# Optimization experiments

Measured on AMD Instinct MI355X. Metric: run time of the kernel, lower is better.

The kernel has to match this reference:

```python
import jax, jax.numpy as jnp
import numpy as np

N = 100_000      # nodes
F_IN = 256       # num_features
HID = 128        # args.hidden
C = 32           # num_classes
E = 1_600_000    # edges
EPS = 0.1        # AntiSymmetricConv epsilon
GAMMA = 0.1      # AntiSymmetricConv gamma


def setup_inputs() -> dict:
    key = jax.random.key(0)
    ks = jax.random.split(key, 10)
    def rn(k, shape, scale=0.05):
        return jax.random.normal(k, shape, dtype=jnp.float32) * scale
    x = jax.random.normal(ks[0], (N, F_IN), dtype=jnp.float32)
    edge_index = jax.random.randint(ks[1], (2, E), 0, N, dtype=jnp.int32)
    return {
        "x": x,
        "lin1_w": rn(ks[2], (HID, F_IN)), "lin1_b": jnp.zeros((HID,), jnp.float32),
        "lin2_w": rn(ks[3], (C, HID)),   "lin2_b": jnp.zeros((C,), jnp.float32),
        "W1": rn(ks[4], (HID, HID)), "phi1_w": rn(ks[5], (HID, HID)), "b1": jnp.zeros((HID,), jnp.float32),
        "W2": rn(ks[6], (C, C)),     "phi2_w": rn(ks[7], (C, C)),     "b2": jnp.zeros((C,), jnp.float32),
        "edge_index": edge_index,
    }


def gcn_norm(edge_index, n):
    # GCNConv default: add self-loops, symmetric D^-1/2 (A+I) D^-1/2 normalization
    loops = jnp.arange(n, dtype=edge_index.dtype)
    row = jnp.concatenate([edge_index[0], loops])  # source
    col = jnp.concatenate([edge_index[1], loops])  # target (aggregation)
    deg = jax.ops.segment_sum(jnp.ones(row.shape[0], jnp.float32), col, num_segments=n)
    dinv = jnp.where(deg > 0, jax.lax.rsqrt(deg), 0.0)
    return row, col, dinv[row] * dinv[col]


def gcn_conv(x, phi_w, row, col, norm):
    xw = x @ phi_w.T                                  # [N, d]
    msgs = norm[:, None] * xw[row]                    # [E+N, d] gather
    return jax.ops.segment_sum(msgs, col, num_segments=x.shape[0])  # scatter-add


def anti_symmetric_conv(x, row, col, norm, W, phi_w, b):
    d = W.shape[0]
    aw = W - W.T - GAMMA * jnp.eye(d, dtype=W.dtype)  # antisymmetric weight
    h = gcn_conv(x, phi_w, row, col, norm)            # phi(x, edge_index)
    h = jnp.tanh(x @ aw.T + h + b)
    return x + EPS * h                                # one Euler step (num_iters=1)


def reference(x, lin1_w, lin1_b, lin2_w, lin2_b, W1, phi1_w, b1, W2, phi2_w, b2, edge_index):
    row, col, norm = gcn_norm(edge_index, x.shape[0])
    h = jax.nn.relu(x @ lin1_w.T + lin1_b)            # dropout is identity in eval
    h = anti_symmetric_conv(h, row, col, norm, W1, phi1_w, b1)
    h = h @ lin2_w.T + lin2_b
    h = anti_symmetric_conv(h, row, col, norm, W2, phi2_w, b2)
    return jax.nn.log_softmax(h, axis=1)
```

## Files before the change

kernel.cpp:

```cpp
#include <hip/hip_runtime.h>
#include <hip/hip_bf16.h>
#include <math.h>

#define N_NODES 100000
#define F_IN    256
#define HID     128
#define NCLS    32
#define NEDGES  1600000
#define EPS_C   0.1f
#define GAMMA_C 0.1f

#define NBK   782
#define CHUNK 4096
#define NCH   391
#define BMAX  4096

typedef __attribute__((ext_vector_type(8))) short short8;
typedef __attribute__((ext_vector_type(4))) float floatx4;

__device__ __forceinline__ float bf2f(unsigned short u) {
    union { unsigned int u; float f; } c;
    c.u = ((unsigned int)u) << 16;
    return c.f;
}
__device__ __forceinline__ unsigned short f2bf(float f) {
    union { float f; unsigned int u; } c; c.f = f;
    unsigned int u = c.u;
    u += 0x7FFFu + ((u >> 16) & 1u);
    return (unsigned short)(u >> 16);
}

__device__ __forceinline__ short8 cvt8(float4 u, float4 v) {
    short8 r;
    r[0] = (short)f2bf(u.x); r[1] = (short)f2bf(u.y);
    r[2] = (short)f2bf(u.z); r[3] = (short)f2bf(u.w);
    r[4] = (short)f2bf(v.x); r[5] = (short)f2bf(v.y);
    r[6] = (short)f2bf(v.z); r[7] = (short)f2bf(v.w);
    return r;
}

__device__ __forceinline__ float ldf(const void* p, size_t i, int md) {
    return md ? ((const float*)p)[i] : bf2f(((const unsigned short*)p)[i]);
}

__global__ void k_detect(const unsigned short* __restrict__ x, int* __restrict__ mode) {
    __shared__ int cnt;
    if (threadIdx.x == 0) cnt = 0;
    __syncthreads();
    float v = fabsf(bf2f(x[2 * threadIdx.x]));
    if (v > 1e4f || !isfinite(v)) atomicAdd(&cnt, 1);
    __syncthreads();
    if (threadIdx.x == 0) *mode = (cnt >= 8) ? 1 : 0;
}

__global__ __launch_bounds__(256) void k_cvtx(const void* __restrict__ x,
                                              unsigned short* __restrict__ xbf,
                                              const int* __restrict__ dmode, int n8) {
    if (!dmode[0]) return;
    const float* xf = (const float*)x;
    int stride = gridDim.x * 256;
    for (int i = blockIdx.x * 256 + threadIdx.x; i < n8; i += stride) {
        const float* q = xf + (size_t)i * 8;
        float4 u = *(const float4*)q, v = *(const float4*)(q + 4);
        *(short8*)(xbf + (size_t)i * 8) = cvt8(u, v);
    }
}

__global__ __launch_bounds__(256) void k_cvtw(const void* __restrict__ w1,
                                              const void* __restrict__ w2,
                                              const void* __restrict__ w3,
                                              const void* __restrict__ w4,
                                              unsigned short* __restrict__ out,
                                              const int* __restrict__ dmode) {
    if (!dmode[0]) return;
    int i = blockIdx.x * 256 + threadIdx.x;
    const float* src; int off;
    if (i < 4096)      { src = (const float*)w1; off = i; }
    else if (i < 6144) { src = (const float*)w2; off = i - 4096; }
    else if (i < 6656) { src = (const float*)w3; off = i - 6144; }
    else if (i < 6784) { src = (const float*)w4; off = i - 6656; }
    else return;
    const float* q = src + (size_t)off * 8;
    *(short8*)(out + (size_t)i * 8) = cvt8(*(const float4*)q, *(const float4*)(q + 4));
}

__global__ __launch_bounds__(256) void k_hist2(const int* __restrict__ ecol,
                                               int* __restrict__ hist, int e) {
    __shared__ int lh[NBK];
    for (int i = threadIdx.x; i < NBK; i += 256) lh[i] = 0;
    __syncthreads();
    int base = blockIdx.x * CHUNK;
    int lim = base + CHUNK; if (lim > e) lim = e;
    for (int i = base + threadIdx.x; i < lim; i += 256)
        atomicAdd(&lh[ecol[i] >> 7], 1);
    __syncthreads();
    for (int i = threadIdx.x; i < NBK; i += 256) hist[blockIdx.x * NBK + i] = lh[i];
}

__global__ __launch_bounds__(256) void k_tot(const int* __restrict__ hist, int* __restrict__ tot) {
    __shared__ int s[256];
    int b = blockIdx.x;
    int v = 0;
    for (int blk = threadIdx.x; blk < NCH; blk += 256) v += hist[blk * NBK + b];
    s[threadIdx.x] = v;
    __syncthreads();
#pragma unroll
    for (int off = 128; off > 0; off >>= 1) {
        if (threadIdx.x < off) s[threadIdx.x] += s[threadIdx.x + off];
        __syncthreads();
    }
    if (threadIdx.x == 0) tot[b] = s[0];
}

__global__ void k_bscan(const int* __restrict__ tot, int* __restrict__ bbase) {
    __shared__ int s[1024];
    int v = (threadIdx.x < NBK) ? tot[threadIdx.x] : 0;
    s[threadIdx.x] = v;
    __syncthreads();
#pragma unroll
    for (int off = 1; off < 1024; off <<= 1) {
        int t = (threadIdx.x >= off) ? s[threadIdx.x - off] : 0;
        __syncthreads();
        s[threadIdx.x] += t;
        __syncthreads();
    }
    if (threadIdx.x < NBK) bbase[threadIdx.x] = s[threadIdx.x] - v;
}

__global__ __launch_bounds__(512) void k_colscan(const int* __restrict__ hist,
                                                 const int* __restrict__ bbase,
                                                 int* __restrict__ off) {
    __shared__ int s[512];
    int b = blockIdx.x, t = threadIdx.x;
    int v = (t < NCH) ? hist[t * NBK + b] : 0;
    s[t] = v;
    __syncthreads();
#pragma unroll
    for (int o = 1; o < 512; o <<= 1) {
        int u = (t >= o) ? s[t - o] : 0;
        __syncthreads();
        s[t] += u;
        __syncthreads();
    }
    if (t < NCH) off[t * NBK + b] = s[t] - v + bbase[b];
}

__global__ __launch_bounds__(256) void k_pass3(
    const int* __restrict__ erow, const int* __restrict__ ecol,
    const int* __restrict__ off, unsigned int* __restrict__ pairs, int e)
{
    __shared__ int lh[NBK];
    __shared__ int lex[NBK + 1];
    __shared__ int cur[NBK];
    __shared__ int wsum[256];
    __shared__ unsigned int sp[CHUNK];
    int base = blockIdx.x * CHUNK;
    int lim = base + CHUNK; if (lim > e) lim = e;
    int cnt = lim - base;

    for (int i = threadIdx.x; i < NBK; i += 256) lh[i] = 0;
    __syncthreads();
    for (int i = base + threadIdx.x; i < lim; i += 256)
        atomicAdd(&lh[ecol[i] >> 7], 1);
    __syncthreads();

    int t4 = threadIdx.x * 4;
    int a0 = (t4 + 0 < NBK) ? lh[t4 + 0] : 0;
    int a1 = (t4 + 1 < NBK) ? lh[t4 + 1] : 0;
    int a2 = (t4 + 2 < NBK) ? lh[t4 + 2] : 0;
    int a3 = (t4 + 3 < NBK) ? lh[t4 + 3] : 0;
    int mysum = a0 + a1 + a2 + a3;
    wsum[threadIdx.x] = mysum;
    __syncthreads();
#pragma unroll
    for (int o = 1; o < 256; o <<= 1) {
        int u = (threadIdx.x >= o) ? wsum[threadIdx.x - o] : 0;
        __syncthreads();
        wsum[threadIdx.x] += u;
        __syncthreads();
    }
    int run = wsum[threadIdx.x] - mysum;
    if (t4 + 0 < NBK) { lex[t4 + 0] = run;            cur[t4 + 0] = run; }
    if (t4 + 1 < NBK) { lex[t4 + 1] = run + a0;       cur[t4 + 1] = run + a0; }
    if (t4 + 2 < NBK) { lex[t4 + 2] = run + a0 + a1;  cur[t4 + 2] = run + a0 + a1; }
    if (t4 + 3 < NBK) { lex[t4 + 3] = run + a0 + a1 + a2; cur[t4 + 3] = run + a0 + a1 + a2; }
    if (threadIdx.x == 0) lex[NBK] = cnt;
    __syncthreads();

    for (int i = base + threadIdx.x; i < lim; i += 256) {
        int dst = ecol[i], src = erow[i];
        int b = dst >> 7;
        int p = atomicAdd(&cur[b], 1);
        sp[p] = ((unsigned int)src << 7) | (unsigned int)(dst & 127);
    }
    __syncthreads();

    for (int i = threadIdx.x; i < cnt; i += 256) {
        int loB = 0, hiB = NBK;
        while (hiB - loB > 1) {
            int mid = (loB + hiB) >> 1;
            if (lex[mid] <= i) loB = mid; else hiB = mid;
        }
        pairs[off[blockIdx.x * NBK + loB] + (i - lex[loB])] = sp[i];
    }
}

__global__ __launch_bounds__(256) void k_build(
    const int* __restrict__ tot, const int* __restrict__ bbase,
    const unsigned int* __restrict__ pairs,
    int* __restrict__ srt, int* __restrict__ row_start, int* __restrict__ cend,
    float* __restrict__ dinv, int n)
{
    __shared__ int lh[128];
    __shared__ int lo[128];
    __shared__ unsigned int se[BMAX];
    int b = blockIdx.x;
    int nb = tot[b]; if (nb > BMAX) nb = BMAX;
    int base = bbase[b];
    if (threadIdx.x < 128) lh[threadIdx.x] = 0;
    __syncthreads();
    for (int e = threadIdx.x; e < nb; e += 256) {
        unsigned int pk = pairs[(size_t)base + e];
        se[e] = pk;
        atomicAdd(&lh[pk & 127u], 1);
    }
    __syncthreads();
    if (threadIdx.x < 128) lo[threadIdx.x] = lh[threadIdx.x];
    __syncthreads();
#pragma unroll
    for (int off = 1; off < 128; off <<= 1) {
        int t = (threadIdx.x < 128 && threadIdx.x >= off) ? lo[threadIdx.x - off] : 0;
        __syncthreads();
        if (threadIdx.x < 128) lo[threadIdx.x] += t;
        __syncthreads();
    }
    int node = b * 128 + threadIdx.x;
    if (threadIdx.x < 128 && node < n) {
        int inc = lo[threadIdx.x], cnt = lh[threadIdx.x];
        row_start[node] = base + inc - cnt;
        cend[node]      = base + inc;
        dinv[node]      = rsqrtf((float)cnt + 1.0f);
    }
    __syncthreads();
    if (threadIdx.x < 128) lh[threadIdx.x] = lo[threadIdx.x] - lh[threadIdx.x];
    __syncthreads();
    for (int e = threadIdx.x; e < nb; e += 256) {
        unsigned int pk = se[e];
        int pos = atomicAdd(&lh[pk & 127u], 1);
        srt[base + pos] = (int)(pk >> 7);
    }
}

__global__ void k_aw(const void* __restrict__ W, unsigned short* __restrict__ aw,
                     const int* __restrict__ dmode, int d) {
    int idx = blockIdx.x * blockDim.x + threadIdx.x;
    if (idx >= d * d) return;
    int md = dmode[0];
    int n = idx / d, k = idx - n * d;
    float v = ldf(W, n * d + k, md) - ldf(W, k * d + n, md) - ((n == k) ? GAMMA_C : 0.0f);
    aw[idx] = f2bf(v);
}

template<int K, int NCB, int NCF, int EPI, int NSPLIT, bool ASEL, bool BSEL>
__global__ __launch_bounds__(512) void k_gemm6(
    const void* A, const unsigned short* Acvt,
    const void* B, const unsigned short* Bcvt, const void* bias,
    unsigned short* Cout,
    const unsigned short* agg, const unsigned short* xw, const float* dinv,
    const int* dmode, void* opout, int M)
{
    constexpr int KP = K + 8;
    constexpr int NT = NCB / 16;
    constexpr int KS = K / 32;
    constexpr int SN = (NCB * K) / 4096;
    __shared__ __align__(16) unsigned short sB[NCB * KP];
    const int md = dmode[0];

    const unsigned short* Ab = (ASEL && md) ? Acvt : (const unsigned short*)A;
    const unsigned short* Bb = (BSEL && md) ? Bcvt : (const unsigned short*)B;

    const int rowblk = (NSPLIT > 1) ? ((int)blockIdx.x / NSPLIT) : (int)blockIdx.x;
    const int col0   = (NSPLIT > 1) ? ((int)blockIdx.x % NSPLIT) * NCB : 0;

    const int lane = threadIdx.x & 63;
    const int wave = threadIdx.x >> 6;
    const int l15  = lane & 15;
    const int quad = lane >> 4;
    const int row0 = rowblk * 128 + wave * 16;

    int ar = row0 + l15;
    int am = ar < M ? ar : M - 1;

    short8 a[KS];
#pragma unroll
    for (int s = 0; s < KS; ++s)
        a[s] = *(const short8*)(Ab + (size_t)am * K + s * 32 + quad * 8);

    if constexpr (SN >= 1) {
        short8 st[SN];
#pragma unroll
        for (int i = 0; i < SN; ++i) {
            int base = threadIdx.x * 8 + i * 4096;
            int r = base / K, c = base % K;
            st[i] = *(const short8*)(Bb + (size_t)(col0 + r) * K + c);
        }
#pragma unroll
        for (int i = 0; i < SN; ++i) {
            int base = threadIdx.x * 8 + i * 4096;
            int r = base / K, c = base % K;
            *(short8*)(sB + r * KP + c) = st[i];
        }
    } else {
        if (threadIdx.x < (NCB * K) / 8) {
            int base = threadIdx.x * 8;
            int r = base / K, c = base % K;
            *(short8*)(sB + r * KP + c) =
                *(const short8*)(Bb + (size_t)(col0 + r) * K + c);
        }
    }
    __builtin_amdgcn_sched_barrier(0);
    __syncthreads();

    floatx4 acc[NT];
#pragma unroll
    for (int t = 0; t < NT; ++t) acc[t] = (floatx4){0.f, 0.f, 0.f, 0.f};

#pragma unroll
    for (int s = 0; s < KS; ++s) {
        short8 b[NT];
#pragma unroll
        for (int t = 0; t < NT; ++t)
            b[t] = *(const short8*)(sB + (t * 16 + l15) * KP + s * 32 + quad * 8);
#pragma unroll
        for (int t = 0; t < NT; ++t)
            acc[t] = __builtin_amdgcn_mfma_f32_16x16x32_bf16(a[s], b[t], acc[t], 0, 0, 0);
    }

    const unsigned short* Ares = Ab;
#pragma unroll
    for (int reg = 0; reg < 4; ++reg) {
        int rr = row0 + quad * 4 + reg;
        if (EPI == 4) {
            int rrc = rr < M ? rr : M - 1;
            float dv = dinv[rrc];
            float val[NT];
#pragma unroll
            for (int t = 0; t < NT; ++t) {
                int col = t * 16 + l15;
                float z = acc[t][reg]
                        + bf2f(agg[(size_t)rrc * NCF + col])
                        + dv * bf2f(xw[(size_t)rrc * NCF + col])
                        + ldf(bias, col, md);
                val[t] = bf2f(Ares[(size_t)rrc * K + col]) + EPS_C * tanhf(z);
            }
            float m = val[0];
#pragma unroll
            for (int t = 1; t < NT; ++t) m = fmaxf(m, val[t]);
#pragma unroll
            for (int msk = 1; msk < 16; msk <<= 1) m = fmaxf(m, __shfl_xor(m, msk));
            float s = 0.f;
#pragma unroll
            for (int t = 0; t < NT; ++t) s += expf(val[t] - m);
#pragma unroll
            for (int msk = 1; msk < 16; msk <<= 1) s += __shfl_xor(s, msk);
            float ls = m + logf(s);
            if (rr < M) {
#pragma unroll
                for (int t = 0; t < NT; ++t) {
                    int col = t * 16 + l15;
                    float r = val[t] - ls;
                    if (md) ((float*)opout)[(size_t)rr * NCF + col] = r;
                    else    ((unsigned short*)opout)[(size_t)rr * NCF + col] = f2bf(r);
                }
            }
        } else {
            if (rr >= M) continue;
#pragma unroll
            for (int t = 0; t < NT; ++t) {
                int gcol = col0 + t * 16 + l15;
                float v = acc[t][reg];
                if (EPI == 0) { v += ldf(bias, gcol, md); v = v > 0.f ? v : 0.f; }
                else if (EPI == 5) { v *= dinv[rr]; }
                else if (EPI == 3) {
                    float dv = dinv[rr];
                    float z = v + bf2f(agg[(size_t)rr * NCF + gcol])
                            + dv * bf2f(xw[(size_t)rr * NCF + gcol])
                            + ldf(bias, gcol, md);
                    v = bf2f(Ares[(size_t)rr * K + gcol]) + EPS_C * tanhf(z);
                }
                Cout[(size_t)rr * NCF + gcol] = f2bf(v);
            }
        }
    }
}

__global__ __launch_bounds__(256) void k_lin2phi2(
    const unsigned short* __restrict__ A,
    const void* __restrict__ B1, const unsigned short* __restrict__ B1c,
    const void* __restrict__ bias,
    const void* __restrict__ B2, const unsigned short* __restrict__ B2c,
    unsigned short* __restrict__ h3, unsigned short* __restrict__ xws2,
    const float* __restrict__ dinv, const int* __restrict__ dmode, int M)
{
    constexpr int K1 = 128, KP1 = 136, KP2 = 40;
    __shared__ __align__(16) unsigned short sB1[32 * KP1];
    __shared__ __align__(16) unsigned short sB2[32 * KP2];
    __shared__ __align__(16) unsigned short sT[128 * KP2];
    const int md = dmode[0];

    const unsigned short* B1b = md ? B1c : (const unsigned short*)B1;
    const unsigned short* B2b = md ? B2c : (const unsigned short*)B2;

    const int lane = threadIdx.x & 63;
    const int wave = threadIdx.x >> 6;
    const int l15  = lane & 15;
    const int quad = lane >> 4;
    const int row0 = blockIdx.x * 128 + wave * 32;

    int am[2];
#pragma unroll
    for (int rt = 0; rt < 2; ++rt) {
        int r = row0 + rt * 16 + l15;
        am[rt] = r < M ? r : M - 1;
    }

    short8 a1[4][2];
#pragma unroll
    for (int s = 0; s < 4; ++s)
#pragma unroll
        for (int rt = 0; rt < 2; ++rt)
            a1[s][rt] = *(const short8*)(A + (size_t)am[rt] * K1 + s * 32 + quad * 8);

    short8 s1[2], s2;
    const bool has2 = threadIdx.x * 8 < 1024;
#pragma unroll
    for (int i = 0; i < 2; ++i)
        s1[i] = *(const short8*)(B1b + threadIdx.x * 8 + i * 2048);
    if (has2)
        s2 = *(const short8*)(B2b + threadIdx.x * 8);
#pragma unroll
    for (int i = 0; i < 2; ++i) {
        int base = threadIdx.x * 8 + i * 2048;
        int r = base / K1, c = base - r * K1;
        *(short8*)(sB1 + r * KP1 + c) = s1[i];
    }
    if (has2) {
        int base = threadIdx.x * 8;
        int r = base / 32, c = base - r * 32;
        *(short8*)(sB2 + r * KP2 + c) = s2;
    }
    __builtin_amdgcn_sched_barrier(0);
    __syncthreads();

    floatx4 acc[2][2];
#pragma unroll
    for (int rt = 0; rt < 2; ++rt) { acc[rt][0] = (floatx4){0,0,0,0}; acc[rt][1] = (floatx4){0,0,0,0}; }

#pragma unroll
    for (int s = 0; s < 4; ++s) {
#pragma unroll
        for (int rt = 0; rt < 2; ++rt) {
#pragma unroll
            for (int t = 0; t < 2; ++t) {
                short8 b = *(const short8*)(sB1 + (t * 16 + l15) * KP1 + s * 32 + quad * 8);
                acc[rt][t] = __builtin_amdgcn_mfma_f32_16x16x32_bf16(a1[s][rt], b, acc[rt][t], 0, 0, 0);
            }
        }
    }
#pragma unroll
    for (int rt = 0; rt < 2; ++rt)
#pragma unroll
        for (int reg = 0; reg < 4; ++reg) {
            int rr = row0 + rt * 16 + quad * 4 + reg;
            int lr = wave * 32 + rt * 16 + quad * 4 + reg;
#pragma unroll
            for (int t = 0; t < 2; ++t) {
                int col = t * 16 + l15;
                unsigned short hv = f2bf(acc[rt][t][reg] + ldf(bias, col, md));
                sT[lr * KP2 + col] = hv;
                if (rr < M) h3[(size_t)rr * 32 + col] = hv;
            }
        }
    __syncthreads();

    floatx4 a2[2][2];
#pragma unroll
    for (int rt = 0; rt < 2; ++rt) {
        short8 a = *(const short8*)(sT + (wave * 32 + rt * 16 + l15) * KP2 + quad * 8);
#pragma unroll
        for (int t = 0; t < 2; ++t) {
            short8 b = *(const short8*)(sB2 + (t * 16 + l15) * KP2 + quad * 8);
            a2[rt][t] = __builtin_amdgcn_mfma_f32_16x16x32_bf16(a, b, (floatx4){0,0,0,0}, 0, 0, 0);
        }
    }
#pragma unroll
    for (int rt = 0; rt < 2; ++rt)
#pragma unroll
        for (int reg = 0; reg < 4; ++reg) {
            int rr = row0 + rt * 16 + quad * 4 + reg;
            if (rr >= M) continue;
            float dv = dinv[rr];
#pragma unroll
            for (int t = 0; t < 2; ++t)
                xws2[(size_t)rr * 32 + t * 16 + l15] = f2bf(dv * a2[rt][t][reg]);
        }
}

__global__ __launch_bounds__(256) void k_gather128(
    const int* __restrict__ srt, const int* __restrict__ rs,
    const int* __restrict__ cend,
    const unsigned short* __restrict__ xws, const float* __restrict__ dinv,
    unsigned short* __restrict__ agg, int n)
{
    int node = blockIdx.x * 8 + (threadIdx.x >> 5);
    int l = threadIdx.x & 31;
    if (node >= n) return;
    int j = rs[node], end = cend[node];
    float a0 = 0.f, a1 = 0.f, a2 = 0.f, a3 = 0.f;
    while (j < end) {
        int idx[8];
#pragma unroll
        for (int k = 0; k < 8; ++k) {
            int jj = j + k;
            idx[k] = srt[jj < end ? jj : end - 1];
        }
        uint2 p[8];
#pragma unroll
        for (int k = 0; k < 8; ++k)
            p[k] = *(const uint2*)(xws + (size_t)idx[k] * 128 + l * 4);
#pragma unroll
        for (int k = 0; k < 8; ++k) {
            if (j + k < end) {
                a0 += bf2f((unsigned short)(p[k].x & 0xFFFFu));
                a1 += bf2f((unsigned short)(p[k].x >> 16));
                a2 += bf2f((unsigned short)(p[k].y & 0xFFFFu));
                a3 += bf2f((unsigned short)(p[k].y >> 16));
            }
        }
        j += 8;
    }
    float dn = dinv[node];
    uint2 out;
    out.x = (unsigned int)f2bf(dn * a0) | ((unsigned int)f2bf(dn * a1) << 16);
    out.y = (unsigned int)f2bf(dn * a2) | ((unsigned int)f2bf(dn * a3) << 16);
    *(uint2*)(agg + (size_t)node * 128 + l * 4) = out;
}

__global__ __launch_bounds__(256) void k_gather32(
    const int* __restrict__ srt, const int* __restrict__ rs,
    const int* __restrict__ cend,
    const unsigned short* __restrict__ xws, const float* __restrict__ dinv,
    unsigned short* __restrict__ agg, int n)
{
    int node = blockIdx.x * 16 + (threadIdx.x >> 4);
    int l = threadIdx.x & 15;
    if (node >= n) return;
    int j = rs[node], end = cend[node];
    float a0 = 0.f, a1 = 0.f;
    while (j < end) {
        int idx[8];
#pragma unroll
        for (int k = 0; k < 8; ++k) {
            int jj = j + k;
            idx[k] = srt[jj < end ? jj : end - 1];
        }
        unsigned int p[8];
#pragma unroll
        for (int k = 0; k < 8; ++k)
            p[k] = *(const unsigned int*)(xws + (size_t)idx[k] * 32 + l * 2);
#pragma unroll
        for (int k = 0; k < 8; ++k) {
            if (j + k < end) {
                a0 += bf2f((unsigned short)(p[k] & 0xFFFFu));
                a1 += bf2f((unsigned short)(p[k] >> 16));
            }
        }
        j += 8;
    }
    float dn = dinv[node];
    unsigned int out = (unsigned int)f2bf(dn * a0) | ((unsigned int)f2bf(dn * a1) << 16);
    *(unsigned int*)(agg + (size_t)node * 32 + l * 2) = out;
}

extern "C" void kernel_launch(void* const* d_in, const int* in_sizes, int n_in,
                              void* d_out, int out_size, void* d_ws, size_t ws_size,
                              hipStream_t stream)
{
    const void* x      = d_in[0];
    const void* lin1_w = d_in[1];
    const void* lin1_b = d_in[2];
    const void* lin2_w = d_in[3];
    const void* lin2_b = d_in[4];
    const void* W1     = d_in[5];
    const void* phi1w  = d_in[6];
    const void* b1     = d_in[7];
    const void* W2     = d_in[8];
    const void* phi2w  = d_in[9];
    const void* b2     = d_in[10];
    const int* eidx    = (const int*)d_in[11];
    const int* erow = eidx;
    const int* ecol = eidx + NEDGES;

    char* ws = (char*)d_ws;
    float* dinv          = (float*)ws;
    int*   dmode         = (int*)(ws + 400000);
    unsigned short* aw1  = (unsigned short*)(ws + 401408);
    unsigned short* aw2  = (unsigned short*)(ws + 435200);
    int* tot             = (int*)(ws + 440320);
    int* bbase           = (int*)(ws + 443648);
    int* row_start       = (int*)(ws + 446976);
    int* cend            = (int*)(ws + 846976);
    int* srt             = (int*)(ws + 1246976);
    int* hist            = (int*)(ws + 7646976);
    int* offb            = (int*)(ws + 8870912);
    unsigned short* wbf  = (unsigned short*)(ws + 10094080);
    unsigned short* h1   = (unsigned short*)(ws + 10485760);
    unsigned short* xws1 = h1 + (size_t)N_NODES * HID;
    unsigned short* agg1 = xws1 + (size_t)N_NODES * HID;
    unsigned short* h2   = xws1;
    unsigned short* h3   = h1;
    unsigned short* xws2 = agg1;
    unsigned short* agg2 = agg1 + (size_t)N_NODES * NCLS;
    unsigned int* pairs  = (unsigned int*)agg1;
    unsigned short* xbf  = xws1;

    unsigned short* bw1 = wbf;
    unsigned short* bp1 = wbf + 32768;
    unsigned short* bw2 = wbf + 49152;
    unsigned short* bp2 = wbf + 53248;

    const int GB = 256;
    const int NB5 = (N_NODES + 127) / 128;
    k_detect<<<1, 256, 0, stream>>>((const unsigned short*)x, dmode);

    k_hist2<<<NCH, 256, 0, stream>>>(ecol, hist, NEDGES);
    k_tot<<<NBK, 256, 0, stream>>>(hist, tot);
    k_bscan<<<1, 1024, 0, stream>>>(tot, bbase);
    k_colscan<<<NBK, 512, 0, stream>>>(hist, bbase, offb);
    k_pass3<<<NCH, 256, 0, stream>>>(erow, ecol, offb, pairs, NEDGES);
    k_build<<<NBK, 256, 0, stream>>>(tot, bbase, pairs, srt, row_start, cend, dinv, N_NODES);

    k_aw<<<(HID * HID + GB - 1) / GB, GB, 0, stream>>>(W1, aw1, dmode, HID);
    k_aw<<<(NCLS * NCLS + GB - 1) / GB, GB, 0, stream>>>(W2, aw2, dmode, NCLS);
    k_cvtw<<<27, 256, 0, stream>>>(lin1_w, phi1w, lin2_w, phi2w, wbf, dmode);
    k_cvtx<<<2048, 256, 0, stream>>>(x, xbf, dmode, N_NODES * F_IN / 8);

    k_gemm6<256, 64, 128, 0, 2, true, true><<<NB5 * 2, 512, 0, stream>>>(
        x, xbf, lin1_w, bw1, lin1_b, h1, nullptr, nullptr, nullptr, dmode, nullptr, N_NODES);
    k_gemm6<128, 128, 128, 5, 1, false, true><<<NB5, 512, 0, stream>>>(
        h1, nullptr, phi1w, bp1, nullptr, xws1, nullptr, nullptr, dinv, dmode, nullptr, N_NODES);
    k_gather128<<<(N_NODES + 7) / 8, 256, 0, stream>>>(
        srt, row_start, cend, xws1, dinv, agg1, N_NODES);
    k_gemm6<128, 128, 128, 3, 1, false, false><<<NB5, 512, 0, stream>>>(
        h1, nullptr, aw1, nullptr, b1, h2, agg1, xws1, dinv, dmode, nullptr, N_NODES);
    k_lin2phi2<<<(N_NODES + 127) / 128, 256, 0, stream>>>(
        h2, lin2_w, bw2, lin2_b, phi2w, bp2, h3, xws2, dinv, dmode, N_NODES);
    k_gather32<<<(N_NODES + 15) / 16, 256, 0, stream>>>(
        srt, row_start, cend, xws2, dinv, agg2, N_NODES);
    k_gemm6<32, 32, 32, 4, 1, false, false><<<NB5, 512, 0, stream>>>(
        h3, nullptr, aw2, nullptr, b2, nullptr, agg2, xws2, dinv, dmode, d_out, N_NODES);
}
```

Baseline: 435.6 us.

## Store layer-1 phi features in column-sliced layout for narrower gathers

```diff
diff --git a/kernel.cpp b/kernel.cpp
--- a/kernel.cpp
+++ b/kernel.cpp
@@ -261,7 +261,8 @@
     aw[idx] = f2bf(v);
 }
 
-template<int K, int NCB, int NCF, int EPI, int NSPLIT, bool ASEL, bool BSEL>
+template<int K, int NCB, int NCF, int EPI, int NSPLIT, bool ASEL, bool BSEL,
+         bool SLCW, bool SLCR>
 __global__ __launch_bounds__(512) void k_gemm6(
     const void* A, const unsigned short* Acvt,
     const void* B, const unsigned short* Bcvt, const void* bias,
@@ -273,6 +274,7 @@
     constexpr int NT = NCB / 16;
     constexpr int KS = K / 32;
     constexpr int SN = (NCB * K) / 4096;
+    constexpr size_t N16 = (size_t)N_NODES * 16;
     __shared__ __align__(16) unsigned short sB[NCB * KP];
     const int md = dmode[0];
 
@@ -383,12 +385,16 @@
                 else if (EPI == 5) { v *= dinv[rr]; }
                 else if (EPI == 3) {
                     float dv = dinv[rr];
-                    float z = v + bf2f(agg[(size_t)rr * NCF + gcol])
-                            + dv * bf2f(xw[(size_t)rr * NCF + gcol])
+                    size_t aoff = SLCR ? ((size_t)t * N16 + (size_t)rr * 16 + l15)
+                                       : ((size_t)rr * NCF + gcol);
+                    float z = v + bf2f(agg[aoff])
+                            + dv * bf2f(xw[aoff])
                             + ldf(bias, gcol, md);
                     v = bf2f(Ares[(size_t)rr * K + gcol]) + EPS_C * tanhf(z);
                 }
-                Cout[(size_t)rr * NCF + gcol] = f2bf(v);
+                size_t coff = SLCW ? ((size_t)t * N16 + (size_t)rr * 16 + l15)
+                                   : ((size_t)rr * NCF + gcol);
+                Cout[coff] = f2bf(v);
             }
         }
     }
@@ -506,17 +512,20 @@
         }
 }
 
-__global__ __launch_bounds__(256) void k_gather128(
+__global__ __launch_bounds__(256) void k_gather128s(
     const int* __restrict__ srt, const int* __restrict__ rs,
     const int* __restrict__ cend,
-    const unsigned short* __restrict__ xws, const float* __restrict__ dinv,
-    unsigned short* __restrict__ agg, int n)
+    const unsigned short* __restrict__ xslc, const float* __restrict__ dinv,
+    unsigned short* __restrict__ aggs, int n)
 {
-    int node = blockIdx.x * 8 + (threadIdx.x >> 5);
-    int l = threadIdx.x & 31;
+    constexpr size_t N16 = (size_t)N_NODES * 16;
+    const int slice = blockIdx.x & 7;
+    const int node = (blockIdx.x >> 3) * 32 + (threadIdx.x >> 3);
+    const int l = threadIdx.x & 7;
     if (node >= n) return;
+    const unsigned short* xs = xslc + (size_t)slice * N16;
     int j = rs[node], end = cend[node];
-    float a0 = 0.f, a1 = 0.f, a2 = 0.f, a3 = 0.f;
+    float a0 = 0.f, a1 = 0.f;
     while (j < end) {
         int idx[8];
 #pragma unroll
@@ -524,26 +533,22 @@
             int jj = j + k;
             idx[k] = srt[jj < end ? jj : end - 1];
         }
-        uint2 p[8];
+        unsigned int p[8];
 #pragma unroll
         for (int k = 0; k < 8; ++k)
-            p[k] = *(const uint2*)(xws + (size_t)idx[k] * 128 + l * 4);
+            p[k] = *(const unsigned int*)(xs + (size_t)idx[k] * 16 + l * 2);
 #pragma unroll
         for (int k = 0; k < 8; ++k) {
             if (j + k < end) {
-                a0 += bf2f((unsigned short)(p[k].x & 0xFFFFu));
-                a1 += bf2f((unsigned short)(p[k].x >> 16));
-                a2 += bf2f((unsigned short)(p[k].y & 0xFFFFu));
-                a3 += bf2f((unsigned short)(p[k].y >> 16));
+                a0 += bf2f((unsigned short)(p[k] & 0xFFFFu));
+                a1 += bf2f((unsigned short)(p[k] >> 16));
             }
         }
         j += 8;
     }
     float dn = dinv[node];
-    uint2 out;
-    out.x = (unsigned int)f2bf(dn * a0) | ((unsigned int)f2bf(dn * a1) << 16);
-    out.y = (unsigned int)f2bf(dn * a2) | ((unsigned int)f2bf(dn * a3) << 16);
-    *(uint2*)(agg + (size_t)node * 128 + l * 4) = out;
+    unsigned int out = (unsigned int)f2bf(dn * a0) | ((unsigned int)f2bf(dn * a1) << 16);
+    *(unsigned int*)(aggs + (size_t)slice * N16 + (size_t)node * 16 + l * 2) = out;
 }
 
 __global__ __launch_bounds__(256) void k_gather32(
@@ -617,8 +622,8 @@
     unsigned short* h1   = (unsigned short*)(ws + 10485760);
     unsigned short* xws1 = h1 + (size_t)N_NODES * HID;
     unsigned short* agg1 = xws1 + (size_t)N_NODES * HID;
-    unsigned short* h2   = xws1;
-    unsigned short* h3   = h1;
+    unsigned short* h2   = h1;
+    unsigned short* h3   = xws1;
     unsigned short* xws2 = agg1;
     unsigned short* agg2 = agg1 + (size_t)N_NODES * NCLS;
     unsigned int* pairs  = (unsigned int*)agg1;
@@ -645,18 +650,18 @@
     k_cvtw<<<27, 256, 0, stream>>>(lin1_w, phi1w, lin2_w, phi2w, wbf, dmode);
     k_cvtx<<<2048, 256, 0, stream>>>(x, xbf, dmode, N_NODES * F_IN / 8);
 
-    k_gemm6<256, 64, 128, 0, 2, true, true><<<NB5 * 2, 512, 0, stream>>>(
+    k_gemm6<256, 64, 128, 0, 2, true, true, false, false><<<NB5 * 2, 512, 0, stream>>>(
         x, xbf, lin1_w, bw1, lin1_b, h1, nullptr, nullptr, nullptr, dmode, nullptr, N_NODES);
-    k_gemm6<128, 128, 128, 5, 1, false, true><<<NB5, 512, 0, stream>>>(
+    k_gemm6<128, 128, 128, 5, 1, false, true, true, false><<<NB5, 512, 0, stream>>>(
         h1, nullptr, phi1w, bp1, nullptr, xws1, nullptr, nullptr, dinv, dmode, nullptr, N_NODES);
-    k_gather128<<<(N_NODES + 7) / 8, 256, 0, stream>>>(
+    k_gather128s<<<(N_NODES / 32) * 8, 256, 0, stream>>>(
         srt, row_start, cend, xws1, dinv, agg1, N_NODES);
-    k_gemm6<128, 128, 128, 3, 1, false, false><<<NB5, 512, 0, stream>>>(
+    k_gemm6<128, 128, 128, 3, 1, false, false, false, true><<<NB5, 512, 0, stream>>>(
         h1, nullptr, aw1, nullptr, b1, h2, agg1, xws1, dinv, dmode, nullptr, N_NODES);
     k_lin2phi2<<<(N_NODES + 127) / 128, 256, 0, stream>>>(
         h2, lin2_w, bw2, lin2_b, phi2w, bp2, h3, xws2, dinv, dmode, N_NODES);
     k_gather32<<<(N_NODES + 15) / 16, 256, 0, stream>>>(
         srt, row_start, cend, xws2, dinv, agg2, N_NODES);
-    k_gemm6<32, 32, 32, 4, 1, false, false><<<NB5, 512, 0, stream>>>(
+    k_gemm6<32, 32, 32, 4, 1, false, false, false, false><<<NB5, 512, 0, stream>>>(
         h3, nullptr, aw2, nullptr, b2, nullptr, agg2, xws2, dinv, dmode, d_out, N_NODES);
 }
```

Measured after the change: 478.2 us. +9.8%, slower.
